# Performance work log

Hardware: AMD Instinct MI355X
Metric: run time of the kernel (lower is better)

The kernel has to match this reference:

```python
import jax, jax.numpy as jnp
import numpy as np

B, I, H, E, V, T = 512, 2560, 512, 300, 8000, 16
SOS = 2

def setup_inputs() -> dict:
    key = jax.random.key(0)
    ks = jax.random.split(key, 12)
    s = lambda k, shape: (jax.random.normal(k, shape, jnp.float32) * 0.05)
    emb = s(ks[2], (V, E)).at[0].set(0.0)  # padding_idx=0
    return dict(
        fused_features=jax.random.normal(ks[0], (B, I), jnp.float32),
        target_answers=jax.random.randint(ks[1], (B, T), 0, V),
        max_len=T,
        embedding=emb,
        W_in=s(ks[3], (H, I)), b_in=jnp.zeros((H,), jnp.float32),
        W_cell=s(ks[4], (H, I)), b_cell=jnp.zeros((H,), jnp.float32),
        W_ih0=s(ks[5], (4 * H, E + H)), W_hh0=s(ks[6], (4 * H, H)),
        b_ih0=jnp.zeros((4 * H,), jnp.float32), b_hh0=jnp.zeros((4 * H,), jnp.float32),
        W_ih1=s(ks[7], (4 * H, H)), W_hh1=s(ks[8], (4 * H, H)),
        b_ih1=jnp.zeros((4 * H,), jnp.float32), b_hh1=jnp.zeros((4 * H,), jnp.float32),
        W_out=s(ks[9], (V, H)), b_out=jnp.zeros((V,), jnp.float32),
    )

def _cell(gates, c):
    # PyTorch LSTM gate order: i, f, g, o
    i, f, g, o = jnp.split(gates, 4, axis=-1)
    c_new = jax.nn.sigmoid(f) * c + jax.nn.sigmoid(i) * jnp.tanh(g)
    h_new = jax.nn.sigmoid(o) * jnp.tanh(c_new)
    return h_new, c_new

def reference(fused_features, target_answers, max_len, embedding,
              W_in, b_in, W_cell, b_cell,
              W_ih0, W_hh0, b_ih0, b_hh0,
              W_ih1, W_hh1, b_ih1, b_hh1,
              W_out, b_out):
    context = fused_features @ W_in.T + b_in          # [B,H]
    cell0 = fused_features @ W_cell.T + b_cell        # [B,H]
    # teacher forcing (ratio=1.0, deterministic): inputs = [SOS, y_0..y_{T-2}]
    words = jnp.concatenate(
        [jnp.full((context.shape[0], 1), SOS, target_answers.dtype),
         target_answers[:, :-1]], axis=1)             # [B,T]
    emb = embedding[words]                            # [B,T,E]
    x = jnp.concatenate(
        [emb, jnp.broadcast_to(context[:, None, :], (emb.shape[0], emb.shape[1], context.shape[1]))],
        axis=-1)                                      # [B,T,E+H]
    # precompute input-side gates for layer 0 in one big GEMM
    xg0 = jnp.einsum('bti,gi->tbg', x, W_ih0) + b_ih0 + b_hh0  # [T,B,4H]

    def step(carry, xg):
        h0, c0, h1, c1 = carry
        h0, c0 = _cell(xg + h0 @ W_hh0.T, c0)
        h1, c1 = _cell(h0 @ W_ih1.T + b_ih1 + b_hh1 + h1 @ W_hh1.T, c1)
        return (h0, c0, h1, c1), h1

    init = (context, cell0, context, cell0)
    _, hs = jax.lax.scan(step, init, xg0)             # hs: [T,B,H]
    logits = jnp.einsum('tbh,vh->btv', hs, W_out) + b_out  # [B,T,V]
    return logits
```

## Files before the change

kernel.cpp:

```cpp
#include <hip/hip_runtime.h>
#include <cstdint>

#define B_   512
#define I_   2560
#define H_   512
#define E_   300
#define EW   320
#define V_   8000
#define VPAD 8064
#define T_   16
#define G4H  2048
#define SOS_ 2

typedef _Float16 f16;
typedef _Float16 f16x8 __attribute__((ext_vector_type(8)));
typedef _Float16 f16x4 __attribute__((ext_vector_type(4)));
typedef float    f32x4 __attribute__((ext_vector_type(4)));

__device__ __forceinline__ float sigmoidf_(float x) {
    return 1.0f / (1.0f + __expf(-x));
}

__device__ __forceinline__ void gload16(const void* g, void* l) {
    __builtin_amdgcn_global_load_lds(
        (const __attribute__((address_space(1))) void*)g,
        (__attribute__((address_space(3))) void*)l,
        16, 0, 0);
}

__global__ __launch_bounds__(256)
void gemm_mfma_f16o(const f16* __restrict__ A, int lda,
                    const f16* __restrict__ Bw, int ldb,
                    f16* __restrict__ C, int ldc,
                    int K,
                    const float* __restrict__ bias1)
{
    __shared__ f16 As[128][32];
    __shared__ f16 Bs[128][32];

    const int tid  = threadIdx.x;
    const int w    = tid >> 6;
    const int lane = tid & 63;
    const int bm   = blockIdx.x * 128;
    const int bn   = blockIdx.y * 128;
    const int wr   = w >> 1;
    const int wc   = w & 1;

    const int srow = lane >> 2;
    const int skel = (lane & 3) * 8;

    const f16* Ag0 = A  + (size_t)(bm + w*32 +      srow) * lda + skel;
    const f16* Ag1 = A  + (size_t)(bm + w*32 + 16 + srow) * lda + skel;
    const f16* Bg0 = Bw + (size_t)(bn + w*32 +      srow) * ldb + skel;
    const f16* Bg1 = Bw + (size_t)(bn + w*32 + 16 + srow) * ldb + skel;
    f16* Al0 = &As[w*32     ][0];
    f16* Al1 = &As[w*32 + 16][0];
    f16* Bl0 = &Bs[w*32     ][0];
    f16* Bl1 = &Bs[w*32 + 16][0];

    const int frow = lane & 15;
    const int fk   = (lane >> 4) * 8;

    f32x4 acc[4][4] = {};

    for (int k0 = 0; k0 < K; k0 += 32) {
        gload16(Ag0 + k0, Al0);
        gload16(Ag1 + k0, Al1);
        gload16(Bg0 + k0, Bl0);
        gload16(Bg1 + k0, Bl1);
        __syncthreads();

        f16x8 af[4], bf[4];
        #pragma unroll
        for (int m = 0; m < 4; ++m)
            af[m] = *reinterpret_cast<const f16x8*>(&As[wr*64 + m*16 + frow][fk]);
        #pragma unroll
        for (int n = 0; n < 4; ++n)
            bf[n] = *reinterpret_cast<const f16x8*>(&Bs[wc*64 + n*16 + frow][fk]);

        #pragma unroll
        for (int m = 0; m < 4; ++m)
            #pragma unroll
            for (int n = 0; n < 4; ++n)
                acc[m][n] = __builtin_amdgcn_mfma_f32_16x16x32_f16(
                    af[m], bf[n], acc[m][n], 0, 0, 0);

        __syncthreads();
    }

    const int rowb = bm + wr*64 + (lane >> 4) * 4;
    #pragma unroll
    for (int n = 0; n < 4; ++n) {
        const int col = bn + wc*64 + n*16 + frow;
        const float badd = bias1 ? bias1[col] : 0.0f;
        #pragma unroll
        for (int m = 0; m < 4; ++m) {
            const int r0 = rowb + m*16;
            #pragma unroll
            for (int r = 0; r < 4; ++r)
                C[(size_t)(r0 + r) * ldc + col] = (f16)(acc[m][n][r] + badd);
        }
    }
}

__global__ __launch_bounds__(256)
void gemm_ctx_init(const f16* __restrict__ A,
                   const f16* __restrict__ Bw,
                   const float* __restrict__ b_in,
                   const float* __restrict__ b_cell,
                   f16* __restrict__ ctx16,
                   f16* __restrict__ h0, f16* __restrict__ h1,
                   float* __restrict__ c0, float* __restrict__ c1)
{
    __shared__ f16 As[128][32];
    __shared__ f16 Bs[128][32];

    const int tid  = threadIdx.x;
    const int w    = tid >> 6;
    const int lane = tid & 63;
    const int bm   = blockIdx.x * 128;
    const int bn   = blockIdx.y * 128;
    const int wr   = w >> 1;
    const int wc   = w & 1;

    const int srow = lane >> 2;
    const int skel = (lane & 3) * 8;

    const f16* Ag0 = A  + (size_t)(bm + w*32 +      srow) * I_ + skel;
    const f16* Ag1 = A  + (size_t)(bm + w*32 + 16 + srow) * I_ + skel;
    const f16* Bg0 = Bw + (size_t)(bn + w*32 +      srow) * I_ + skel;
    const f16* Bg1 = Bw + (size_t)(bn + w*32 + 16 + srow) * I_ + skel;
    f16* Al0 = &As[w*32     ][0];
    f16* Al1 = &As[w*32 + 16][0];
    f16* Bl0 = &Bs[w*32     ][0];
    f16* Bl1 = &Bs[w*32 + 16][0];

    const int frow = lane & 15;
    const int fk   = (lane >> 4) * 8;

    f32x4 acc[4][4] = {};

    for (int k0 = 0; k0 < I_; k0 += 32) {
        gload16(Ag0 + k0, Al0);
        gload16(Ag1 + k0, Al1);
        gload16(Bg0 + k0, Bl0);
        gload16(Bg1 + k0, Bl1);
        __syncthreads();

        f16x8 af[4], bf[4];
        #pragma unroll
        for (int m = 0; m < 4; ++m)
            af[m] = *reinterpret_cast<const f16x8*>(&As[wr*64 + m*16 + frow][fk]);
        #pragma unroll
        for (int n = 0; n < 4; ++n)
            bf[n] = *reinterpret_cast<const f16x8*>(&Bs[wc*64 + n*16 + frow][fk]);

        #pragma unroll
        for (int m = 0; m < 4; ++m)
            #pragma unroll
            for (int n = 0; n < 4; ++n)
                acc[m][n] = __builtin_amdgcn_mfma_f32_16x16x32_f16(
                    af[m], bf[n], acc[m][n], 0, 0, 0);

        __syncthreads();
    }

    const int rowb = bm + wr*64 + (lane >> 4) * 4;
    #pragma unroll
    for (int n = 0; n < 4; ++n) {
        const int col = bn + wc*64 + n*16 + frow;
        #pragma unroll
        for (int m = 0; m < 4; ++m) {
            const int r0 = rowb + m*16;
            #pragma unroll
            for (int r = 0; r < 4; ++r) {
                const int row = r0 + r;
                if (col < 512) {
                    const f16 ch = (f16)(acc[m][n][r] + b_in[col]);
                    ctx16[(size_t)row * 512 + col] = ch;
                    h0[(size_t)row * 512 + col] = ch;
                    h1[(size_t)row * 512 + col] = ch;
                } else {
                    const float cc = acc[m][n][r] + b_cell[col - 512];
                    c0[(size_t)row * 512 + col - 512] = cc;
                    c1[(size_t)row * 512 + col - 512] = cc;
                }
            }
        }
    }
}

__device__ __forceinline__ void gemm_cell_body(
    const f16* __restrict__ Ap1, const f16* __restrict__ Ap2, int lda2,
    const f16* __restrict__ Wp, int K,
    const f16* __restrict__ Cadd,
    const float* __restrict__ bih, const float* __restrict__ bhh,
    float* __restrict__ cst,
    f16* __restrict__ hout1,
    char* smem, int bm, int bn)
{
    const int tid  = threadIdx.x;
    const int w    = tid >> 6;
    const int lane = tid & 63;
    const int wr   = w >> 1, wc = w & 1;
    const int frow = lane & 15, hi = lane >> 4;
    const int sw   = (frow & 7) << 4;
    const int srow8 = lane >> 3;
    const int ksb  = ((((lane & 7) * 16) ^ (srow8 << 4)) >> 1);

    const int NT = K >> 6;
    f32x4 acc[2][4] = {};

    char* Abuf = smem;
    char* Wbuf = smem + 24576;

    auto stage = [&](int bsel, int kt) {
        const int k0 = kt << 6;
        #pragma unroll
        for (int j = 0; j < 2; ++j) {
            const int row = w*16 + j*8 + srow8;
            const f16* src;
            if (k0 < 512) src = Ap1 + (size_t)(bm + row) * 512  + k0 + ksb;
            else          src = Ap2 + (size_t)(bm + row) * lda2 + (k0 - 512) + ksb;
            gload16(src, Abuf + bsel*8192 + (w*2 + j)*1024 + lane*16);
        }
        #pragma unroll
        for (int j = 0; j < 4; ++j) {
            const int row = w*32 + j*8 + srow8;
            gload16(Wp + (size_t)(bn + row) * K + k0 + ksb,
                    Wbuf + bsel*16384 + (w*4 + j)*1024 + lane*16);
        }
    };

    stage(0, 0);
    stage(1, 1);

    int rb = 0;
    for (int kt = 0; kt < NT; ++kt) {
        if (kt < NT - 1) asm volatile("s_waitcnt vmcnt(6)" ::: "memory");
        else             asm volatile("s_waitcnt vmcnt(0)" ::: "memory");
        __builtin_amdgcn_sched_barrier(0);
        __builtin_amdgcn_s_barrier();
        __builtin_amdgcn_sched_barrier(0);

        const char* A_ = Abuf + rb*8192;
        const char* W_ = Wbuf + rb*16384;
        f16x8 af[2][2], bf[2][4];
        #pragma unroll
        for (int ks = 0; ks < 2; ++ks) {
            const int cb = (ks*64 + hi*16) ^ sw;
            #pragma unroll
            for (int m = 0; m < 2; ++m)
                af[ks][m] = *reinterpret_cast<const f16x8*>(A_ + (wr*32 + m*16 + frow)*128 + cb);
            #pragma unroll
            for (int n = 0; n < 4; ++n)
                bf[ks][n] = *reinterpret_cast<const f16x8*>(W_ + (wc*64 + n*16 + frow)*128 + cb);
        }

        if (kt + 2 < NT) {
            int sb = rb - 1; if (sb < 0) sb = 2;
            stage(sb, kt + 2);
        }

        #pragma unroll
        for (int ks = 0; ks < 2; ++ks)
            #pragma unroll
            for (int m = 0; m < 2; ++m)
                #pragma unroll
                for (int n = 0; n < 4; ++n)
                    acc[m][n] = __builtin_amdgcn_mfma_f32_16x16x32_f16(
                        af[ks][m], bf[ks][n], acc[m][n], 0, 0, 0);
        rb = (rb == 2) ? 0 : rb + 1;
    }
    __syncthreads();

    float* gs = (float*)smem;
    #pragma unroll
    for (int m = 0; m < 2; ++m) {
        const int row = wr*32 + m*16 + hi*4;
        #pragma unroll
        for (int n = 0; n < 4; ++n) {
            const int col = wc*64 + n*16 + frow;
            #pragma unroll
            for (int r = 0; r < 4; ++r) {
                float v = acc[m][n][r];
                if (Cadd) v += (float)Cadd[(size_t)(bm + row + r) * G4H + bn + col];
                gs[(row + r)*132 + col] = v;
            }
        }
    }
    __syncthreads();

    const int hp = tid & 31;
    const int hg = (bn >> 2) + hp;
    float bi0 = 0.f, bi1 = 0.f, bi2 = 0.f, bi3 = 0.f;
    if (bih) {
        bi0 = bih[hg]        + bhh[hg];
        bi1 = bih[512 + hg]  + bhh[512 + hg];
        bi2 = bih[1024 + hg] + bhh[1024 + hg];
        bi3 = bih[1536 + hg] + bhh[1536 + hg];
    }
    #pragma unroll
    for (int i = 0; i < 8; ++i) {
        const int r = (tid >> 5) * 8 + i;
        const int b = bm + r;
        const float gi = gs[r*132 +      hp] + bi0;
        const float gf = gs[r*132 + 32 + hp] + bi1;
        const float gc = gs[r*132 + 64 + hp] + bi2;
        const float go = gs[r*132 + 96 + hp] + bi3;
        const float c  = cst[(size_t)b * 512 + hg];
        const float cn = sigmoidf_(gf) * c + sigmoidf_(gi) * tanhf(gc);
        const float hn = sigmoidf_(go) * tanhf(cn);
        cst[(size_t)b * 512 + hg] = cn;
        hout1[(size_t)b * 512 + hg] = (f16)hn;
    }
}

__device__ __forceinline__ void gemm_out_body(
    const f16* __restrict__ A, const f16* __restrict__ Bw,
    float* __restrict__ C,
    const float* __restrict__ bias,
    int bm, int bn, char* smem, int tid)
{
    const int w    = tid >> 6;
    const int lane = tid & 63;
    const int wr   = w >> 1, wc = w & 1;
    const int frow = lane & 15, hi = lane >> 4;
    const int sw   = (frow & 7) << 4;
    const int srow8 = lane >> 3;
    const int ksb  = ((((lane & 7) * 16) ^ (srow8 << 4)) >> 1);

    char* Abuf = smem;
    char* Wbuf = smem + 32768;
    f32x4 acc[4][4] = {};

    auto stage = [&](int bsel, int kt) {
        const int k0 = kt << 6;
        #pragma unroll
        for (int j = 0; j < 4; ++j) {
            const int row = w*32 + j*8 + srow8;
            gload16(A  + (size_t)(bm + row) * 512 + k0 + ksb,
                    Abuf + bsel*16384 + (w*4 + j)*1024 + lane*16);
            gload16(Bw + (size_t)(bn + row) * 512 + k0 + ksb,
                    Wbuf + bsel*16384 + (w*4 + j)*1024 + lane*16);
        }
    };

    stage(0, 0);
    stage(1, 1);

    int buf = 0;
    for (int kt = 0; kt < 8; ++kt) {
        if (kt < 7) asm volatile("s_waitcnt vmcnt(8)" ::: "memory");
        else        asm volatile("s_waitcnt vmcnt(0)" ::: "memory");
        __builtin_amdgcn_sched_barrier(0);
        __builtin_amdgcn_s_barrier();
        __builtin_amdgcn_sched_barrier(0);

        const char* A_ = Abuf + buf*16384;
        const char* W_ = Wbuf + buf*16384;
        f16x8 af[2][4], bf[2][4];
        #pragma unroll
        for (int ks = 0; ks < 2; ++ks) {
            const int cb = (ks*64 + hi*16) ^ sw;
            #pragma unroll
            for (int m = 0; m < 4; ++m)
                af[ks][m] = *reinterpret_cast<const f16x8*>(A_ + (wr*64 + m*16 + frow)*128 + cb);
            #pragma unroll
            for (int n = 0; n < 4; ++n)
                bf[ks][n] = *reinterpret_cast<const f16x8*>(W_ + (wc*64 + n*16 + frow)*128 + cb);
        }
        __builtin_amdgcn_sched_barrier(0);
        asm volatile("s_waitcnt lgkmcnt(0)" ::: "memory");
        __builtin_amdgcn_sched_barrier(0);
        __builtin_amdgcn_s_barrier();
        __builtin_amdgcn_sched_barrier(0);

        if (kt + 2 < 8) stage(buf, kt + 2);

        #pragma unroll
        for (int ks = 0; ks < 2; ++ks)
            #pragma unroll
            for (int m = 0; m < 4; ++m)
                #pragma unroll
                for (int n = 0; n < 4; ++n)
                    acc[m][n] = __builtin_amdgcn_mfma_f32_16x16x32_f16(
                        af[ks][m], bf[ks][n], acc[m][n], 0, 0, 0);
        buf ^= 1;
    }

    const int rowb = bm + wr*64 + (lane >> 4) * 4;
    #pragma unroll
    for (int n = 0; n < 4; ++n) {
        const int col = bn + wc*64 + n*16 + frow;
        if (col >= V_) continue;
        const float badd = bias[col];
        #pragma unroll
        for (int m = 0; m < 4; ++m) {
            const int r0 = rowb + m*16;
            #pragma unroll
            for (int r = 0; r < 4; ++r)
                __builtin_nontemporal_store(
                    acc[m][n][r] + badd,
                    &C[(size_t)(r0 + r) * (T_ * V_) + col]);
        }
    }
}

__global__ __launch_bounds__(256)
void phase_kernel(const f16* __restrict__ h0in,
                  const f16* __restrict__ embt,
                  f16* __restrict__ h0out,
                  const f16* __restrict__ h1in,
                  f16* __restrict__ h1out,
                  const f16* __restrict__ W0p, const f16* __restrict__ W1p,
                  const f16* __restrict__ WoutP,
                  const f16* __restrict__ ctxg,
                  const float* __restrict__ bih1, const float* __restrict__ bhh1,
                  const float* __restrict__ b_out,
                  float* __restrict__ c0, float* __restrict__ c1,
                  float* __restrict__ out, int tout,
                  int bx0, int active0, int active1, int activeO)
{
    __shared__ char smem[73728];
    const int bx = blockIdx.x + bx0;

    if (bx < 128) {
        if (!active0) return;
        const int xcd = bx & 7, idx = bx >> 3;
        const int bn = (xcd*2 + (idx & 1)) * 128;
        const int bm = (idx >> 1) * 64;
        gemm_cell_body(h0in, embt, EW, W0p, 832,
                       ctxg, nullptr, nullptr, c0, h0out, smem, bm, bn);
    } else if (bx < 256) {
        if (!active1) return;
        const int lb = bx - 128;
        const int xcd = lb & 7, idx = lb >> 3;
        const int bn = (xcd*2 + (idx & 1)) * 128;
        const int bm = (idx >> 1) * 64;
        gemm_cell_body(h0in, h1in, 512, W1p, 1024,
                       nullptr, bih1, bhh1, c1, h1out, smem, bm, bn);
    } else {
        if (!activeO) return;
        const int o = bx - 256;
        const int xcd = o & 7, j = o >> 3;
        const int bnt = xcd*8 + (j >> 2);
        if (bnt >= 63) return;
        const int bm = (j & 3) * 128;
        gemm_out_body(h1in, WoutP, out + (size_t)tout * V_, b_out,
                      bm, bnt * 128, smem, threadIdx.x);
    }
}

#define NB_F16   1280
#define NB_WIC   2560
#define NB_W0    1664
#define NB_W1    2048
#define NB_WCTX  1024
#define NB_B0    8
#define NB_WOUT  4032
#define NB_EMB   2560
#define NB_TOTAL (NB_F16+NB_WIC+NB_W0+NB_W1+NB_WCTX+NB_B0+NB_WOUT+NB_EMB)

__global__ __launch_bounds__(256)
void pack_all(const float* __restrict__ fused,
              const float* __restrict__ Win, const float* __restrict__ Wcell,
              const float* __restrict__ Whh0, const float* __restrict__ Wih0,
              const float* __restrict__ Wih1, const float* __restrict__ Whh1,
              const float* __restrict__ bih0, const float* __restrict__ bhh0,
              const float* __restrict__ Wout,
              const float* __restrict__ emb, const int* __restrict__ target,
              f16* __restrict__ fused16, f16* __restrict__ WinCell,
              f16* __restrict__ W0, f16* __restrict__ W1,
              f16* __restrict__ Wc, float* __restrict__ b01p,
              f16* __restrict__ Wo, f16* __restrict__ embAll)
{
    int bx = blockIdx.x;
    const int tid = threadIdx.x;

    auto cvt4 = [](float4 v) {
        return f16x4{ (f16)v.x, (f16)v.y, (f16)v.z, (f16)v.w };
    };

    if (bx < NB_F16) {
        const int i = bx * 256 + tid;
        *reinterpret_cast<f16x4*>(fused16 + (size_t)i * 4) =
            cvt4(reinterpret_cast<const float4*>(fused)[i]);
        return;
    }
    bx -= NB_F16;
    if (bx < NB_WIC) {
        const int i = bx * 256 + tid;
        const int r = i / 640, c4 = (i % 640) * 4;
        const float* src = (r < 512) ? Win + (size_t)r * I_ + c4
                                     : Wcell + (size_t)(r - 512) * I_ + c4;
        *reinterpret_cast<f16x4*>(WinCell + (size_t)i * 4) =
            cvt4(*reinterpret_cast<const float4*>(src));
        return;
    }
    bx -= NB_WIC;
    if (bx < NB_W0) {
        const int idx = bx * 256 + tid;
        const int rp = idx / 208, k = (idx % 208) * 4;
        const int g = (rp >> 5) & 3, h = (rp >> 7) * 32 + (rp & 31);
        const int srow = g * 512 + h;
        f16x4 o = { (f16)0.f, (f16)0.f, (f16)0.f, (f16)0.f };
        if (k < 512)
            o = cvt4(*reinterpret_cast<const float4*>(Whh0 + (size_t)srow * 512 + k));
        else if (k < 812)
            o = cvt4(*reinterpret_cast<const float4*>(Wih0 + (size_t)srow * 812 + (k - 512)));
        *reinterpret_cast<f16x4*>(W0 + (size_t)rp * 832 + k) = o;
        return;
    }
    bx -= NB_W0;
    if (bx < NB_W1) {
        const int idx = bx * 256 + tid;
        const int rp = idx >> 8, k = (idx & 255) * 4;
        const int g = (rp >> 5) & 3, h = (rp >> 7) * 32 + (rp & 31);
        const int srow = g * 512 + h;
        const float* src = (k < 512) ? Wih1 + (size_t)srow * 512 + k
                                     : Whh1 + (size_t)srow * 512 + (k - 512);
        *reinterpret_cast<f16x4*>(W1 + (size_t)rp * 1024 + k) =
            cvt4(*reinterpret_cast<const float4*>(src));
        return;
    }
    bx -= NB_W1;
    if (bx < NB_WCTX) {
        const int idx = bx * 256 + tid;
        const int rp = idx >> 7, k = (idx & 127) * 4;
        const int g = (rp >> 5) & 3, h = (rp >> 7) * 32 + (rp & 31);
        *reinterpret_cast<f16x4*>(Wc + (size_t)rp * 512 + k) =
            cvt4(*reinterpret_cast<const float4*>(
                Wih0 + (size_t)(g * 512 + h) * 812 + 300 + k));
        return;
    }
    bx -= NB_WCTX;
    if (bx < NB_B0) {
        const int idx = bx * 256 + tid;
        const int g = (idx >> 5) & 3, h = (idx >> 7) * 32 + (idx & 31);
        b01p[idx] = bih0[g * 512 + h] + bhh0[g * 512 + h];
        return;
    }
    bx -= NB_B0;
    if (bx < NB_WOUT) {
        const int i = bx * 256 + tid;
        const int r = i >> 7, c4 = (i & 127) * 4;
        f16x4 o = { (f16)0.f, (f16)0.f, (f16)0.f, (f16)0.f };
        if (r < V_)
            o = cvt4(*reinterpret_cast<const float4*>(Wout + (size_t)r * H_ + c4));
        *reinterpret_cast<f16x4*>(Wo + (size_t)i * 4) = o;
        return;
    }
    bx -= NB_WOUT;
    {
        const int idx = bx * 256 + tid;
        const int t = idx / (B_ * 80);
        const int rem = idx % (B_ * 80);
        const int b = rem / 80, e = (rem % 80) * 4;
        const int wd = (t == 0) ? SOS_ : target[b * T_ + (t - 1)];
        f16x4 o = { (f16)0.f, (f16)0.f, (f16)0.f, (f16)0.f };
        if (e < E_)
            o = cvt4(*reinterpret_cast<const float4*>(emb + (size_t)wd * E_ + e));
        *reinterpret_cast<f16x4*>(embAll + ((size_t)t * B_ + b) * EW + e) = o;
    }
}

extern "C" void kernel_launch(void* const* d_in, const int* in_sizes, int n_in,
                              void* d_out, int out_size, void* d_ws, size_t ws_size,
                              hipStream_t stream)
{
    const float* fused  = (const float*)d_in[0];
    const int*   target = (const int*)d_in[1];
    const float* emb    = (const float*)d_in[3];
    const float* W_in   = (const float*)d_in[4];
    const float* b_in   = (const float*)d_in[5];
    const float* W_cell = (const float*)d_in[6];
    const float* b_cell = (const float*)d_in[7];
    const float* W_ih0  = (const float*)d_in[8];
    const float* W_hh0  = (const float*)d_in[9];
    const float* b_ih0  = (const float*)d_in[10];
    const float* b_hh0  = (const float*)d_in[11];
    const float* W_ih1  = (const float*)d_in[12];
    const float* W_hh1  = (const float*)d_in[13];
    const float* b_ih1  = (const float*)d_in[14];
    const float* b_hh1  = (const float*)d_in[15];
    const float* W_out  = (const float*)d_in[16];
    const float* b_out  = (const float*)d_in[17];
    float* out = (float*)d_out;

    char* p = (char*)d_ws;
    auto carve = [&](size_t bytes) {
        char* r = p;
        p += (bytes + 255) & ~(size_t)255;
        return r;
    };
    f16* ctxg     = (f16*)carve((size_t)B_ * G4H * 2);
    float* b01p   = (float*)carve((size_t)G4H * 4);
    float* c0     = (float*)carve((size_t)B_ * H_ * 4);
    float* c1     = (float*)carve((size_t)B_ * H_ * 4);
    f16* fused16  = (f16*)carve((size_t)B_ * I_ * 2);
    f16* WinCell  = (f16*)carve((size_t)1024 * I_ * 2);
    f16* W0p      = (f16*)carve((size_t)G4H * 832 * 2);
    f16* W1p      = (f16*)carve((size_t)G4H * 1024 * 2);
    f16* Wctxp    = (f16*)carve((size_t)G4H * H_ * 2);
    f16* Wout16   = (f16*)carve((size_t)VPAD * H_ * 2);
    f16* ctx16    = (f16*)carve((size_t)B_ * H_ * 2);
    f16* h0a      = (f16*)carve((size_t)B_ * H_ * 2);
    f16* h0b      = (f16*)carve((size_t)B_ * H_ * 2);
    f16* h1a      = (f16*)carve((size_t)B_ * H_ * 2);
    f16* h1b      = (f16*)carve((size_t)B_ * H_ * 2);
    f16* embAll   = (f16*)carve((size_t)T_ * B_ * EW * 2);

    pack_all<<<dim3(NB_TOTAL), 256, 0, stream>>>(
        fused, W_in, W_cell, W_hh0, W_ih0, W_ih1, W_hh1,
        b_ih0, b_hh0, W_out, emb, target,
        fused16, WinCell, W0p, W1p, Wctxp, b01p, Wout16, embAll);

    gemm_ctx_init<<<dim3(B_/128, 1024/128), 256, 0, stream>>>(
        fused16, WinCell, b_in, b_cell, ctx16, h0b, h1b, c0, c1);

    gemm_mfma_f16o<<<dim3(B_/128, G4H/128), 256, 0, stream>>>(
        ctx16, H_, Wctxp, H_, ctxg, G4H, H_, b01p);

    f16* h0buf[2] = { h0a, h0b };
    f16* h1buf[2] = { h1a, h1b };
    for (int phase = 0; phase <= T_ + 1; ++phase) {
        const int a0 = (phase < T_) ? 1 : 0;
        const int a1 = (phase >= 1 && phase <= T_) ? 1 : 0;
        const int aO = (phase >= 2) ? 1 : 0;
        const int te = (phase < T_) ? phase : (T_ - 1);
        const int tO = aO ? (phase - 2) : 0;
        int bx0 = 0, nb = 512;
        if (phase == 0)            { bx0 = 0;   nb = 128; }
        else if (phase == 1)       { bx0 = 0;   nb = 256; }
        else if (phase == T_)      { bx0 = 128; nb = 384; }
        else if (phase == T_ + 1)  { bx0 = 256; nb = 256; }
        phase_kernel<<<dim3(nb), 256, 0, stream>>>(
            h0buf[(phase + 1) & 1],
            embAll + (size_t)te * B_ * EW,
            h0buf[phase & 1],
            h1buf[phase & 1],
            h1buf[(phase + 1) & 1],
            W0p, W1p, Wout16, ctxg, b_ih1, b_hh1, b_out,
            c0, c1, out, tO, bx0, a0, a1, aO);
    }
}
```

Before: 410.0 us.

## Replace per-phase kernel launches with a persistent cooperative kernel using grid sync

```diff
diff --git a/kernel.cpp b/kernel.cpp
--- a/kernel.cpp
+++ b/kernel.cpp
@@ -1,5 +1,8 @@
 #include <hip/hip_runtime.h>
+#include <hip/hip_cooperative_groups.h>
 #include <cstdint>
+
+namespace cg = cooperative_groups;
 
 #define B_   512
 #define I_   2560
@@ -314,6 +317,7 @@
         cst[(size_t)b * 512 + hg] = cn;
         hout1[(size_t)b * 512 + hg] = (f16)hn;
     }
+    __syncthreads();
 }
 
 __device__ __forceinline__ void gemm_out_body(
@@ -404,6 +408,66 @@
                     acc[m][n][r] + badd,
                     &C[(size_t)(r0 + r) * (T_ * V_) + col]);
         }
+    }
+    __syncthreads();
+}
+
+struct PersistArgs {
+    const f16* embAll;
+    const f16* W0p; const f16* W1p; const f16* WoutP;
+    const f16* ctxg;
+    const float* bih1; const float* bhh1; const float* b_out;
+    float* c0; float* c1;
+    f16* h0a; f16* h0b; f16* h1a; f16* h1b;
+    float* out;
+};
+
+__global__ __launch_bounds__(256, 2)
+void lstm_persist(PersistArgs a)
+{
+    __shared__ char smem[73728];
+    cg::grid_group grid = cg::this_grid();
+    const int bx = blockIdx.x;
+    const int tid = threadIdx.x;
+
+    f16* h0buf[2] = { a.h0a, a.h0b };
+    f16* h1buf[2] = { a.h1a, a.h1b };
+
+    for (int p = 0; p <= T_ + 1; ++p) {
+        if (bx < 128) {
+            if (p < T_) {
+                const int xcd = bx & 7, idx = bx >> 3;
+                const int bn = (xcd*2 + (idx & 1)) * 128;
+                const int bm = (idx >> 1) * 64;
+                gemm_cell_body(h0buf[(p + 1) & 1],
+                               a.embAll + (size_t)p * B_ * EW, EW,
+                               a.W0p, 832, a.ctxg, nullptr, nullptr,
+                               a.c0, h0buf[p & 1], smem, bm, bn);
+            }
+        } else if (bx < 256) {
+            if (p >= 1 && p <= T_) {
+                const int lb = bx - 128;
+                const int xcd = lb & 7, idx = lb >> 3;
+                const int bn = (xcd*2 + (idx & 1)) * 128;
+                const int bm = (idx >> 1) * 64;
+                gemm_cell_body(h0buf[(p + 1) & 1],
+                               h1buf[p & 1], 512,
+                               a.W1p, 1024, nullptr, a.bih1, a.bhh1,
+                               a.c1, h1buf[(p + 1) & 1], smem, bm, bn);
+            }
+        } else {
+            if (p >= 2) {
+                const int o = bx - 256;
+                const int xcd = o & 7, j = o >> 3;
+                const int bnt = xcd*8 + (j >> 2);
+                const int bm = (j & 3) * 128;
+                if (bnt < 63)
+                    gemm_out_body(h1buf[p & 1], a.WoutP,
+                                  a.out + (size_t)(p - 2) * V_, a.b_out,
+                                  bm, bnt * 128, smem, tid);
+            }
+        }
+        if (p < T_ + 1) grid.sync();
     }
 }
 
@@ -622,26 +686,47 @@
     gemm_mfma_f16o<<<dim3(B_/128, G4H/128), 256, 0, stream>>>(
         ctx16, H_, Wctxp, H_, ctxg, G4H, H_, b01p);
 
-    f16* h0buf[2] = { h0a, h0b };
-    f16* h1buf[2] = { h1a, h1b };
-    for (int phase = 0; phase <= T_ + 1; ++phase) {
-        const int a0 = (phase < T_) ? 1 : 0;
-        const int a1 = (phase >= 1 && phase <= T_) ? 1 : 0;
-        const int aO = (phase >= 2) ? 1 : 0;
-        const int te = (phase < T_) ? phase : (T_ - 1);
-        const int tO = aO ? (phase - 2) : 0;
-        int bx0 = 0, nb = 512;
-        if (phase == 0)            { bx0 = 0;   nb = 128; }
-        else if (phase == 1)       { bx0 = 0;   nb = 256; }
-        else if (phase == T_)      { bx0 = 128; nb = 384; }
-        else if (phase == T_ + 1)  { bx0 = 256; nb = 256; }
-        phase_kernel<<<dim3(nb), 256, 0, stream>>>(
-            h0buf[(phase + 1) & 1],
-            embAll + (size_t)te * B_ * EW,
-            h0buf[phase & 1],
-            h1buf[phase & 1],
-            h1buf[(phase + 1) & 1],
-            W0p, W1p, Wout16, ctxg, b_ih1, b_hh1, b_out,
-            c0, c1, out, tO, bx0, a0, a1, aO);
-    }
-}
+    PersistArgs pa;
+    pa.embAll = embAll; pa.W0p = W0p; pa.W1p = W1p; pa.WoutP = Wout16;
+    pa.ctxg = ctxg; pa.bih1 = b_ih1; pa.bhh1 = b_hh1; pa.b_out = b_out;
+    pa.c0 = c0; pa.c1 = c1;
+    pa.h0a = h0a; pa.h0b = h0b; pa.h1a = h1a; pa.h1b = h1b;
+    pa.out = out;
+
+    int maxBlk = 0;
+    hipError_t qerr = hipOccupancyMaxActiveBlocksPerMultiprocessor(
+        &maxBlk, (const void*)lstm_persist, 256, 0);
+    bool usePersist = (qerr == hipSuccess && maxBlk >= 2);
+
+    if (usePersist) {
+        void* kargs[] = { (void*)&pa };
+        hipError_t lerr = hipLaunchCooperativeKernel(
+            (const void*)lstm_persist, dim3(512), dim3(256), kargs, 0, stream);
+        usePersist = (lerr == hipSuccess);
+    }
+
+    if (!usePersist) {
+        f16* h0buf[2] = { h0a, h0b };
+        f16* h1buf[2] = { h1a, h1b };
+        for (int phase = 0; phase <= T_ + 1; ++phase) {
+            const int a0 = (phase < T_) ? 1 : 0;
+            const int a1 = (phase >= 1 && phase <= T_) ? 1 : 0;
+            const int aO = (phase >= 2) ? 1 : 0;
+            const int te = (phase < T_) ? phase : (T_ - 1);
+            const int tO = aO ? (phase - 2) : 0;
+            int bx0 = 0, nb = 512;
+            if (phase == 0)            { bx0 = 0;   nb = 128; }
+            else if (phase == 1)       { bx0 = 0;   nb = 256; }
+            else if (phase == T_)      { bx0 = 128; nb = 384; }
+            else if (phase == T_ + 1)  { bx0 = 256; nb = 256; }
+            phase_kernel<<<dim3(nb), 256, 0, stream>>>(
+                h0buf[(phase + 1) & 1],
+                embAll + (size_t)te * B_ * EW,
+                h0buf[phase & 1],
+                h1buf[phase & 1],
+                h1buf[(phase + 1) & 1],
+                W0p, W1p, Wout16, ctxg, b_ih1, b_hh1, b_out,
+                c0, c1, out, tO, bx0, a0, a1, aO);
+        }
+    }
+}
```

New measurement: 410.7 us. About the same (+0.2%).
